# Kernel tuning notes

Hardware: AMD Instinct MI355X
Metric: run time of the kernel (lower is better)

## Reference

```python
import jax, jax.numpy as jnp
import numpy as np

B, T, D, HS = 4, 4096, 1024, 64


def setup_inputs() -> dict:
    key = jax.random.key(0)
    k1, k2, k3 = jax.random.split(key, 3)
    x = jax.random.normal(k1, (B, T, D), dtype=jnp.float32)
    # Linear(n_embd, head_size, bias=False) weights: [head_size, n_embd]
    Wk = jax.random.normal(k2, (HS, D), dtype=jnp.float32) * (D ** -0.5)
    Wv = jax.random.normal(k3, (HS, D), dtype=jnp.float32) * (D ** -0.5)
    return {"x": x, "Wk": Wk, "Wv": Wv}


def reference(x, Wk, Wv):
    # Faithful to source: q = self.value(x) (query proj is dead code), so q and v
    # share the value projection.
    k = jnp.einsum('btd,hd->bth', x, Wk)   # [B,T,HS]
    qv = jnp.einsum('btd,hd->bth', x, Wv)  # [B,T,HS]; serves as both q and v
    scale = k.shape[-1] ** -0.5
    scores = jnp.einsum('bth,bsh->bts', qv, k) * scale  # [B,T,T]
    causal = jnp.tril(jnp.ones((T, T), dtype=bool))
    scores = jnp.where(causal, scores, -jnp.inf)
    weights = jax.nn.softmax(scores, axis=-1)
    out = jnp.einsum('bts,bsh->bth', weights, qv)  # [B,T,HS]
    return out
```

## Files before the change

kernel.cpp:

```cpp
#include <hip/hip_runtime.h>
#include <hip/hip_bf16.h>

typedef __bf16 bf16;
typedef __attribute__((ext_vector_type(4))) __bf16 bf16x4;
typedef __attribute__((ext_vector_type(8))) __bf16 bf16x8;
typedef __attribute__((ext_vector_type(4))) float f32x4;

#define T_SEQ 4096
#define D_EMB 1024
#define HS 64

__device__ __forceinline__ float fexp2(float x) {
#if __has_builtin(__builtin_amdgcn_exp2f)
    return __builtin_amdgcn_exp2f(x);
#else
    return exp2f(x);
#endif
}

__global__ __launch_bounds__(256) void wcast_kernel(
    const float* __restrict__ Wk, const float* __restrict__ Wv,
    bf16* __restrict__ wbf)
{
    const int t = blockIdx.x * 256 + threadIdx.x;
    const int base = t * 8;
    const float* src = (base < 65536) ? (Wk + base) : (Wv + base - 65536);
    float4 f0 = *(const float4*)(src);
    float4 f1 = *(const float4*)(src + 4);
    bf16x8 o = {(__bf16)f0.x, (__bf16)f0.y, (__bf16)f0.z, (__bf16)f0.w,
                (__bf16)f1.x, (__bf16)f1.y, (__bf16)f1.z, (__bf16)f1.w};
    *(bf16x8*)(wbf + base) = o;
}

__global__ __launch_bounds__(256, 2) void proj_kernel(
    const float* __restrict__ x,
    const bf16* __restrict__ wbf,
    bf16* __restrict__ kmat,
    bf16* __restrict__ qvmat,
    bf16* __restrict__ qvT)
{
    __shared__ bf16 xs[32][72];
    __shared__ bf16 wsh[128][72];
    __shared__ bf16 vt[64][40];

    const int tid  = threadIdx.x;
    const int lane = tid & 63;
    const int wave = tid >> 6;
    const int col  = lane & 15;
    const int quad = lane >> 4;
    const int rowbase = blockIdx.x * 32;

    f32x4 acc[2][2];
#pragma unroll
    for (int mt = 0; mt < 2; ++mt)
#pragma unroll
        for (int nt = 0; nt < 2; ++nt) acc[mt][nt] = {0.f, 0.f, 0.f, 0.f};

    float4 xn[2];
    bf16x8 wn[4];
    {
#pragma unroll
        for (int p = 0; p < 2; ++p) {
            const int idx = p * 256 + tid;
            const int xr  = idx >> 4;
            const int c4  = (idx & 15) * 4;
            xn[p] = *(const float4*)(x + (size_t)(rowbase + xr) * D_EMB + c4);
        }
#pragma unroll
        for (int p = 0; p < 4; ++p) {
            const int idx = p * 256 + tid;
            const int wr  = idx >> 3;
            const int off = (idx & 7) * 8;
            wn[p] = *(const bf16x8*)(wbf + (size_t)wr * D_EMB + off);
        }
    }

#pragma unroll 1
    for (int c = 0; c < 16; ++c) {
#pragma unroll
        for (int p = 0; p < 2; ++p) {
            const int idx = p * 256 + tid;
            const int xr  = idx >> 4;
            const int c4  = (idx & 15) * 4;
            bf16x4 v = {(__bf16)xn[p].x, (__bf16)xn[p].y,
                        (__bf16)xn[p].z, (__bf16)xn[p].w};
            *(bf16x4*)&xs[xr][c4] = v;
        }
#pragma unroll
        for (int p = 0; p < 4; ++p) {
            const int idx = p * 256 + tid;
            const int wr  = idx >> 3;
            const int off = (idx & 7) * 8;
            *(bf16x8*)&wsh[wr][off] = wn[p];
        }
        __syncthreads();

        if (c < 15) {
            const int k0 = (c + 1) * 64;
#pragma unroll
            for (int p = 0; p < 2; ++p) {
                const int idx = p * 256 + tid;
                const int xr  = idx >> 4;
                const int c4  = (idx & 15) * 4;
                xn[p] = *(const float4*)(x + (size_t)(rowbase + xr) * D_EMB + k0 + c4);
            }
#pragma unroll
            for (int p = 0; p < 4; ++p) {
                const int idx = p * 256 + tid;
                const int wr  = idx >> 3;
                const int off = (idx & 7) * 8;
                wn[p] = *(const bf16x8*)(wbf + (size_t)wr * D_EMB + k0 + off);
            }
        }

#pragma unroll
        for (int s = 0; s < 2; ++s) {
            bf16x8 af[2];
#pragma unroll
            for (int mt = 0; mt < 2; ++mt)
                af[mt] = *(const bf16x8*)&xs[mt * 16 + col][s * 32 + quad * 8];
            bf16x8 bfr[2];
#pragma unroll
            for (int nt = 0; nt < 2; ++nt)
                bfr[nt] = *(const bf16x8*)&wsh[wave * 32 + nt * 16 + col][s * 32 + quad * 8];
#pragma unroll
            for (int mt = 0; mt < 2; ++mt)
#pragma unroll
                for (int nt = 0; nt < 2; ++nt)
                    acc[mt][nt] = __builtin_amdgcn_mfma_f32_16x16x32_bf16(
                        af[mt], bfr[nt], acc[mt][nt], 0, 0, 0);
        }
        __syncthreads();
    }

#pragma unroll
    for (int mt = 0; mt < 2; ++mt)
#pragma unroll
        for (int nt = 0; nt < 2; ++nt) {
            const int gcol = wave * 32 + nt * 16 + col;
#pragma unroll
            for (int r = 0; r < 4; ++r) {
                const int grow = rowbase + mt * 16 + quad * 4 + r;
                const int ltt  = mt * 16 + quad * 4 + r;
                bf16 bv = (bf16)acc[mt][nt][r];
                if (gcol < 64) {
                    kmat[(size_t)grow * HS + gcol] = bv;
                } else {
                    qvmat[(size_t)grow * HS + (gcol - 64)] = bv;
                    vt[gcol - 64][ltt] = bv;
                }
            }
        }
    __syncthreads();

    {
        const int h   = tid >> 2;
        const int seg = (tid & 3) * 8;
        bf16x8 v = *(const bf16x8*)&vt[h][seg];
        const int bb  = rowbase >> 12;
        const int tt0 = (rowbase & (T_SEQ - 1)) + seg;
        *(bf16x8*)(qvT + ((size_t)bb * HS + h) * T_SEQ + tt0) = v;
    }
}

__global__ __launch_bounds__(256, 4) void attn_kernel(
    const bf16* __restrict__ kmat,
    const bf16* __restrict__ qvmat,
    const bf16* __restrict__ qvT,
    float* __restrict__ out,
    float* __restrict__ o_parts,
    float* __restrict__ l_parts)
{
    __shared__ bf16 Kt[64][72];
    __shared__ bf16 Vt[64][72];
    __shared__ bf16 plds[4][16][40];

    const int tid  = threadIdx.x;
    const int lane = tid & 63;
    const int wave = tid >> 6;
    const int col  = lane & 15;
    const int quad = lane >> 4;

    const int b = blockIdx.x / 288;
    const int r = 287 - (blockIdx.x - b * 288);
    int a = 0;
    while (4 * (a + 1) * (a + 2) <= r) ++a;
    const int rr = r - 4 * a * (a + 1);
    const int m  = rr / (a + 1);
    const int jc = rr - m * (a + 1);
    const int qb = 8 * a + m;

    const int cbeg  = jc * 8;
    const int nctot = qb + 1;
    const int cend  = (nctot < cbeg + 8) ? nctot : cbeg + 8;

    const bf16* qvb = qvmat + (size_t)b * T_SEQ * HS;
    const bf16* kb  = kmat  + (size_t)b * T_SEQ * HS;
    const bf16* vTb = qvT   + (size_t)b * HS * T_SEQ;

    const int q0 = qb * 64 + wave * 16;

    bf16x8 qf0 = *(const bf16x8*)(qvb + (size_t)(q0 + col) * HS + quad * 8);
    bf16x8 qf1 = *(const bf16x8*)(qvb + (size_t)(q0 + col) * HS + 32 + quad * 8);

    f32x4 o[4];
    float lp[4];
#pragma unroll
    for (int h = 0; h < 4; ++h) o[h] = {0.f, 0.f, 0.f, 0.f};
#pragma unroll
    for (int i = 0; i < 4; ++i) lp[i] = 0.f;

    const float sc = 0.125f * 1.44269504088896f;

    bf16x8 kn[2], vn[2];
    {
        const int kc = cbeg * 64;
#pragma unroll
        for (int it = 0; it < 2; ++it) {
            const int idx = it * 256 + tid;
            const int kr  = idx >> 3;
            const int off = (idx & 7) * 8;
            kn[it] = *(const bf16x8*)(kb + (size_t)kc * HS + idx * 8);
            vn[it] = *(const bf16x8*)(vTb + (size_t)kr * T_SEQ + kc + off);
        }
    }

#pragma unroll 1
    for (int c = cbeg; c < cend; ++c) {
#pragma unroll
        for (int it = 0; it < 2; ++it) {
            const int idx = it * 256 + tid;
            const int kr  = idx >> 3;
            const int off = (idx & 7) * 8;
            *(bf16x8*)&Kt[kr][off] = kn[it];
            *(bf16x8*)&Vt[kr][off] = vn[it];
        }
        __syncthreads();

        if (c + 1 < cend) {
            const int kcn = (c + 1) * 64;
#pragma unroll
            for (int it = 0; it < 2; ++it) {
                const int idx = it * 256 + tid;
                const int kr  = idx >> 3;
                const int off = (idx & 7) * 8;
                kn[it] = *(const bf16x8*)(kb + (size_t)kcn * HS + idx * 8);
                vn[it] = *(const bf16x8*)(vTb + (size_t)kr * T_SEQ + kcn + off);
            }
        }

        const int kc = c * 64;
#pragma unroll
        for (int st = 0; st < 2; ++st) {
            const int gk = kc + 32 * st;
            if (gk > q0 + 15) break;

            bf16x8 b0 = *(const bf16x8*)&Kt[32 * st + col][quad * 8];
            bf16x8 b1 = *(const bf16x8*)&Kt[32 * st + col][32 + quad * 8];
            bf16x8 b2 = *(const bf16x8*)&Kt[32 * st + 16 + col][quad * 8];
            bf16x8 b3 = *(const bf16x8*)&Kt[32 * st + 16 + col][32 + quad * 8];

            float p[2][4];
            {
                f32x4 a4 = {0.f, 0.f, 0.f, 0.f};
                a4 = __builtin_amdgcn_mfma_f32_16x16x32_bf16(qf0, b0, a4, 0, 0, 0);
                a4 = __builtin_amdgcn_mfma_f32_16x16x32_bf16(qf1, b1, a4, 0, 0, 0);
#pragma unroll
                for (int i = 0; i < 4; ++i) p[0][i] = fexp2(fmaf(a4[i], sc, -24.f));
            }
            {
                f32x4 a4 = {0.f, 0.f, 0.f, 0.f};
                a4 = __builtin_amdgcn_mfma_f32_16x16x32_bf16(qf0, b2, a4, 0, 0, 0);
                a4 = __builtin_amdgcn_mfma_f32_16x16x32_bf16(qf1, b3, a4, 0, 0, 0);
#pragma unroll
                for (int i = 0; i < 4; ++i) p[1][i] = fexp2(fmaf(a4[i], sc, -24.f));
            }

            if (gk + 31 > q0) {
#pragma unroll
                for (int nt = 0; nt < 2; ++nt)
#pragma unroll
                    for (int i = 0; i < 4; ++i)
                        if (gk + nt * 16 + col > q0 + quad * 4 + i)
                            p[nt][i] = 0.f;
            }

#pragma unroll
            for (int i = 0; i < 4; ++i) lp[i] += p[0][i] + p[1][i];

#pragma unroll
            for (int nt = 0; nt < 2; ++nt)
#pragma unroll
                for (int i = 0; i < 4; ++i)
                    plds[wave][quad * 4 + i][nt * 16 + col] = (bf16)p[nt][i];
            bf16x8 pa = *(const bf16x8*)&plds[wave][col][quad * 8];

#pragma unroll
            for (int h = 0; h < 4; ++h) {
                bf16x8 vb = *(const bf16x8*)&Vt[h * 16 + col][32 * st + quad * 8];
                o[h] = __builtin_amdgcn_mfma_f32_16x16x32_bf16(pa, vb, o[h], 0, 0, 0);
            }
        }
        __syncthreads();
    }

    float lr[4];
#pragma unroll
    for (int i = 0; i < 4; ++i) {
        float v = lp[i];
#pragma unroll
        for (int off = 1; off < 16; off <<= 1)
            v += __shfl_xor(v, off, 64);
        lr[i] = v;
    }

    const size_t rowbase = (size_t)b * T_SEQ + q0 + quad * 4;
    if (col == 0) {
#pragma unroll
        for (int i = 0; i < 4; ++i)
            l_parts[(size_t)jc * 16384 + rowbase + i] = lr[i];
    }

    float* dst = (jc == 0) ? out : (o_parts + (size_t)(jc - 1) * 16384 * HS);
#pragma unroll
    for (int h = 0; h < 4; ++h)
#pragma unroll
        for (int i = 0; i < 4; ++i)
            dst[(rowbase + i) * HS + h * 16 + col] = o[h][i];
}

__global__ __launch_bounds__(256) void norm_kernel(
    float* __restrict__ out,
    const float* __restrict__ o_parts,
    const float* __restrict__ l_parts)
{
    const int i   = blockIdx.x * 256 + threadIdx.x;
    const int row = i >> 6;
    const int qb  = (row & 4095) >> 6;
    const int nj  = (qb >> 3) + 1;

    float s = out[i];
    float L = l_parts[row];
    for (int j = 1; j < nj; ++j) {
        s += o_parts[(size_t)(j - 1) * 1048576 + i];
        L += l_parts[(size_t)j * 16384 + row];
    }
    out[i] = s / L;
}

extern "C" void kernel_launch(void* const* d_in, const int* in_sizes, int n_in,
                              void* d_out, int out_size, void* d_ws, size_t ws_size,
                              hipStream_t stream) {
    const float* x  = (const float*)d_in[0];
    const float* Wk = (const float*)d_in[1];
    const float* Wv = (const float*)d_in[2];
    float* out = (float*)d_out;

    bf16* ws    = (bf16*)d_ws;
    bf16* wbf   = ws;
    bf16* kmat  = ws + (size_t)128 * 1024;
    bf16* qvmat = kmat + (size_t)16384 * 64;
    bf16* qvT   = qvmat + (size_t)16384 * 64;
    float* o_parts = (float*)(qvT + (size_t)16384 * 64);
    float* l_parts = o_parts + (size_t)7 * 16384 * 64;

    wcast_kernel<<<64, 256, 0, stream>>>(Wk, Wv, wbf);
    proj_kernel<<<512, 256, 0, stream>>>(x, wbf, kmat, qvmat, qvT);
    attn_kernel<<<1152, 256, 0, stream>>>(kmat, qvmat, qvT, out, o_parts, l_parts);
    norm_kernel<<<4096, 256, 0, stream>>>(out, o_parts, l_parts);
}
```

Measured before the change: 138.4 us.

## Compute transposed scores so P feeds PV MFMA from registers without LDS

The score MFMA now has its operands swapped, producing S^T. Each lane then holds four consecutive key probabilities for one query, which is exactly the A-operand layout of the 16x16x16 bf16 MFMA. That lets P go straight into the PV multiply and drops the per-step LDS write/read of P along with its buffer. The second 16-key half of a diagonal step is skipped when it lies entirely above the causal boundary, and the row-sum reduction shrinks to two shuffles. The trade-off is that the PV product now uses twice as many half-K MFMAs instead of the 16x16x32 instruction.

```diff
diff --git a/kernel.cpp b/kernel.cpp
--- a/kernel.cpp
+++ b/kernel.cpp
@@ -5,10 +5,17 @@
 typedef __attribute__((ext_vector_type(4))) __bf16 bf16x4;
 typedef __attribute__((ext_vector_type(8))) __bf16 bf16x8;
 typedef __attribute__((ext_vector_type(4))) float f32x4;
+typedef __attribute__((ext_vector_type(4))) short s16x4;
 
 #define T_SEQ 4096
 #define D_EMB 1024
 #define HS 64
+
+#if __has_builtin(__builtin_amdgcn_mfma_f32_16x16x16bf16_1k)
+#define MFMA16_OK 1
+#else
+#define MFMA16_OK 0
+#endif
 
 __device__ __forceinline__ float fexp2(float x) {
 #if __has_builtin(__builtin_amdgcn_exp2f)
@@ -17,6 +24,12 @@
     return exp2f(x);
 #endif
 }
+
+#if MFMA16_OK
+__device__ __forceinline__ s16x4 bc4(bf16x4 v) {
+    return __builtin_bit_cast(s16x4, v);
+}
+#endif
 
 __global__ __launch_bounds__(256) void wcast_kernel(
     const float* __restrict__ Wk, const float* __restrict__ Wv,
@@ -173,7 +186,9 @@
 {
     __shared__ bf16 Kt[64][72];
     __shared__ bf16 Vt[64][72];
+#if !MFMA16_OK
     __shared__ bf16 plds[4][16][40];
+#endif
 
     const int tid  = threadIdx.x;
     const int lane = tid & 63;
@@ -204,11 +219,9 @@
     bf16x8 qf1 = *(const bf16x8*)(qvb + (size_t)(q0 + col) * HS + 32 + quad * 8);
 
     f32x4 o[4];
-    float lp[4];
 #pragma unroll
     for (int h = 0; h < 4; ++h) o[h] = {0.f, 0.f, 0.f, 0.f};
-#pragma unroll
-    for (int i = 0; i < 4; ++i) lp[i] = 0.f;
+    float lsum = 0.f;
 
     const float sc = 0.125f * 1.44269504088896f;
 
@@ -257,70 +270,84 @@
 
             bf16x8 b0 = *(const bf16x8*)&Kt[32 * st + col][quad * 8];
             bf16x8 b1 = *(const bf16x8*)&Kt[32 * st + col][32 + quad * 8];
-            bf16x8 b2 = *(const bf16x8*)&Kt[32 * st + 16 + col][quad * 8];
-            bf16x8 b3 = *(const bf16x8*)&Kt[32 * st + 16 + col][32 + quad * 8];
-
-            float p[2][4];
+
+            float p0[4], p1[4];
             {
                 f32x4 a4 = {0.f, 0.f, 0.f, 0.f};
-                a4 = __builtin_amdgcn_mfma_f32_16x16x32_bf16(qf0, b0, a4, 0, 0, 0);
-                a4 = __builtin_amdgcn_mfma_f32_16x16x32_bf16(qf1, b1, a4, 0, 0, 0);
-#pragma unroll
-                for (int i = 0; i < 4; ++i) p[0][i] = fexp2(fmaf(a4[i], sc, -24.f));
-            }
-            {
+                a4 = __builtin_amdgcn_mfma_f32_16x16x32_bf16(b0, qf0, a4, 0, 0, 0);
+                a4 = __builtin_amdgcn_mfma_f32_16x16x32_bf16(b1, qf1, a4, 0, 0, 0);
+#pragma unroll
+                for (int i = 0; i < 4; ++i) p0[i] = fexp2(fmaf(a4[i], sc, -24.f));
+            }
+            const bool do1 = (gk + 16 <= q0 + 15);
+            if (do1) {
+                bf16x8 b2 = *(const bf16x8*)&Kt[32 * st + 16 + col][quad * 8];
+                bf16x8 b3 = *(const bf16x8*)&Kt[32 * st + 16 + col][32 + quad * 8];
                 f32x4 a4 = {0.f, 0.f, 0.f, 0.f};
-                a4 = __builtin_amdgcn_mfma_f32_16x16x32_bf16(qf0, b2, a4, 0, 0, 0);
-                a4 = __builtin_amdgcn_mfma_f32_16x16x32_bf16(qf1, b3, a4, 0, 0, 0);
-#pragma unroll
-                for (int i = 0; i < 4; ++i) p[1][i] = fexp2(fmaf(a4[i], sc, -24.f));
+                a4 = __builtin_amdgcn_mfma_f32_16x16x32_bf16(b2, qf0, a4, 0, 0, 0);
+                a4 = __builtin_amdgcn_mfma_f32_16x16x32_bf16(b3, qf1, a4, 0, 0, 0);
+#pragma unroll
+                for (int i = 0; i < 4; ++i) p1[i] = fexp2(fmaf(a4[i], sc, -24.f));
+            } else {
+#pragma unroll
+                for (int i = 0; i < 4; ++i) p1[i] = 0.f;
             }
 
             if (gk + 31 > q0) {
 #pragma unroll
-                for (int nt = 0; nt < 2; ++nt)
+                for (int i = 0; i < 4; ++i)
+                    if (gk + quad * 4 + i > q0 + col) p0[i] = 0.f;
+                if (do1) {
 #pragma unroll
                     for (int i = 0; i < 4; ++i)
-                        if (gk + nt * 16 + col > q0 + quad * 4 + i)
-                            p[nt][i] = 0.f;
-            }
-
-#pragma unroll
-            for (int i = 0; i < 4; ++i) lp[i] += p[0][i] + p[1][i];
-
-#pragma unroll
-            for (int nt = 0; nt < 2; ++nt)
-#pragma unroll
-                for (int i = 0; i < 4; ++i)
-                    plds[wave][quad * 4 + i][nt * 16 + col] = (bf16)p[nt][i];
+                        if (gk + 16 + quad * 4 + i > q0 + col) p1[i] = 0.f;
+                }
+            }
+
+            lsum += (p0[0] + p0[1]) + (p0[2] + p0[3]);
+            if (do1) lsum += (p1[0] + p1[1]) + (p1[2] + p1[3]);
+
+#if MFMA16_OK
+            bf16x4 pa0 = {(bf16)p0[0], (bf16)p0[1], (bf16)p0[2], (bf16)p0[3]};
+            s16x4 pa0s = bc4(pa0);
+#pragma unroll
+            for (int h = 0; h < 4; ++h) {
+                bf16x4 vb = *(const bf16x4*)&Vt[h * 16 + col][32 * st + quad * 4];
+                o[h] = __builtin_amdgcn_mfma_f32_16x16x16bf16_1k(
+                    pa0s, bc4(vb), o[h], 0, 0, 0);
+            }
+            if (do1) {
+                bf16x4 pa1 = {(bf16)p1[0], (bf16)p1[1], (bf16)p1[2], (bf16)p1[3]};
+                s16x4 pa1s = bc4(pa1);
+#pragma unroll
+                for (int h = 0; h < 4; ++h) {
+                    bf16x4 vb = *(const bf16x4*)&Vt[h * 16 + col][32 * st + 16 + quad * 4];
+                    o[h] = __builtin_amdgcn_mfma_f32_16x16x16bf16_1k(
+                        pa1s, bc4(vb), o[h], 0, 0, 0);
+                }
+            }
+#else
+            bf16x4 w0 = {(bf16)p0[0], (bf16)p0[1], (bf16)p0[2], (bf16)p0[3]};
+            bf16x4 w1 = {(bf16)p1[0], (bf16)p1[1], (bf16)p1[2], (bf16)p1[3]};
+            *(bf16x4*)&plds[wave][col][quad * 4]      = w0;
+            *(bf16x4*)&plds[wave][col][16 + quad * 4] = w1;
             bf16x8 pa = *(const bf16x8*)&plds[wave][col][quad * 8];
-
 #pragma unroll
             for (int h = 0; h < 4; ++h) {
                 bf16x8 vb = *(const bf16x8*)&Vt[h * 16 + col][32 * st + quad * 8];
                 o[h] = __builtin_amdgcn_mfma_f32_16x16x32_bf16(pa, vb, o[h], 0, 0, 0);
             }
+#endif
         }
         __syncthreads();
     }
 
-    float lr[4];
-#pragma unroll
-    for (int i = 0; i < 4; ++i) {
-        float v = lp[i];
-#pragma unroll
-        for (int off = 1; off < 16; off <<= 1)
-            v += __shfl_xor(v, off, 64);
-        lr[i] = v;
-    }
+    lsum += __shfl_xor(lsum, 16, 64);
+    lsum += __shfl_xor(lsum, 32, 64);
+    if (quad == 0)
+        l_parts[(size_t)jc * 16384 + (size_t)b * T_SEQ + q0 + col] = lsum;
 
     const size_t rowbase = (size_t)b * T_SEQ + q0 + quad * 4;
-    if (col == 0) {
-#pragma unroll
-        for (int i = 0; i < 4; ++i)
-            l_parts[(size_t)jc * 16384 + rowbase + i] = lr[i];
-    }
-
     float* dst = (jc == 0) ? out : (o_parts + (size_t)(jc - 1) * 16384 * HS);
 #pragma unroll
     for (int h = 0; h < 4; ++h)
```

New measurement: 137.4 us. No clear change (-0.8%).
